# Kernel optimization log

Hardware: AMD Instinct MI355X
Metric: run time of the kernel (lower is better)

## Reference

```python
import jax, jax.numpy as jnp
import numpy as np

B, T, I, H, C = 128, 1024, 256, 512, 10


def setup_inputs() -> dict:
    key = jax.random.key(0)
    ks = jax.random.split(key, 11)
    s1 = 1.0 / np.sqrt(H)
    u = lambda k, shp, s: jax.random.uniform(k, shp, jnp.float32, -s, s)
    return {
        "x": jax.random.normal(ks[0], (B, T, I), jnp.float32),
        "w_ih1": u(ks[1], (H, I), s1),
        "w_hh1": u(ks[2], (H, H), s1),
        "b_ih1": u(ks[3], (H,), s1),
        "b_hh1": u(ks[4], (H,), s1),
        "w_ih2": u(ks[5], (H, H), s1),
        "w_hh2": u(ks[6], (H, H), s1),
        "b_ih2": u(ks[7], (H,), s1),
        "b_hh2": u(ks[8], (H,), s1),
        "w_out": u(ks[9], (C, H), s1),
        "b_out": u(ks[10], (C,), s1),
    }


def reference(x, w_ih1, w_hh1, b_ih1, b_hh1, w_ih2, w_hh2, b_ih2, b_hh2, w_out, b_out):
    batch = x.shape[0]
    h0 = jnp.zeros((batch, H), x.dtype)

    def step(carry, x_t):
        h1, h2 = carry
        # cell 1: tanh(x_t @ w_ih1^T + b_ih1 + h1 @ w_hh1^T + b_hh1)
        h1 = jnp.tanh(x_t @ w_ih1.T + b_ih1 + h1 @ w_hh1.T + b_hh1)
        # cell 2 takes h1 as input
        h2 = jnp.tanh(h1 @ w_ih2.T + b_ih2 + h2 @ w_hh2.T + b_hh2)
        return (h1, h2), None

    # scan over time: x transposed to [T, B, I]
    (h1_T, h2_T), _ = jax.lax.scan(step, (h0, h0), jnp.swapaxes(x, 0, 1))
    return h2_T @ w_out.T + b_out
```

## Files before the change

kernel.cpp:

```cpp
#include <hip/hip_runtime.h>
#include <hip/hip_fp16.h>

#define Tt 1024
#define Ii 256
#define Hh 512
#define Cc 10
#define SPINMAX (1 << 27)

typedef _Float16 f16;
typedef _Float16 f16x8 __attribute__((ext_vector_type(8)));
typedef _Float16 f16x4 __attribute__((ext_vector_type(4)));
typedef _Float16 f16x2 __attribute__((ext_vector_type(2)));
typedef float    f32x4 __attribute__((ext_vector_type(4)));

#define OFF_FLAGS 0u
#define OFF_WH1   4096u
#define OFF_WH2   528384u
#define OFF_XWR   1052672u
#define OFF_H1R   3149824u
#define OFF_PAR   4198400u

static __device__ __forceinline__ f32x4 mfma16(f16x8 a, f16x8 b, f32x4 c) {
  return __builtin_amdgcn_mfma_f32_16x16x32_f16(a, b, c, 0, 0, 0);
}
static __device__ __forceinline__ float fast_tanh(float v) {
  float e = __expf(2.0f * v);
  return 1.0f - 2.0f / (e + 1.0f);
}
static __device__ __forceinline__ int ldflag(const int* p) {
  return __hip_atomic_load(p, __ATOMIC_RELAXED, __HIP_MEMORY_SCOPE_AGENT);
}
static __device__ __forceinline__ void stflag(int* p, int v) {
  __hip_atomic_store(p, v, __ATOMIC_RELAXED, __HIP_MEMORY_SCOPE_AGENT);
}
static __device__ __forceinline__ f16x4 ld64cc(const f16* p) {
  union { unsigned long long u; f16x4 v; } U;
  U.u = __hip_atomic_load((const unsigned long long*)p, __ATOMIC_RELAXED, __HIP_MEMORY_SCOPE_AGENT);
  return U.v;
}
static __device__ __forceinline__ void st64cc(f16* p, f16x4 v) {
  union { unsigned long long u; f16x4 v; } U; U.v = v;
  __hip_atomic_store((unsigned long long*)p, U.u, __ATOMIC_RELAXED, __HIP_MEMORY_SCOPE_AGENT);
}
static __device__ __forceinline__ f16x8 ld128cc(const f16* p) {
  union { unsigned long long u[2]; f16x8 v; } U;
  U.u[0] = __hip_atomic_load((const unsigned long long*)p,     __ATOMIC_RELAXED, __HIP_MEMORY_SCOPE_AGENT);
  U.u[1] = __hip_atomic_load((const unsigned long long*)p + 1, __ATOMIC_RELAXED, __HIP_MEMORY_SCOPE_AGENT);
  return U.v;
}
static __device__ __forceinline__ void stu32cc(unsigned* p, unsigned v) {
  __hip_atomic_store(p, v, __ATOMIC_RELAXED, __HIP_MEMORY_SCOPE_AGENT);
}
static __device__ __forceinline__ int imin(int a, int b) { return a < b ? a : b; }

#define CFENCE() asm volatile("" ::: "memory")
#define VMFENCE() asm volatile("s_waitcnt vmcnt(0)" ::: "memory")
#define LBAR() do { asm volatile("s_waitcnt lgkmcnt(0)" ::: "memory"); \
                    __builtin_amdgcn_s_barrier(); \
                    __builtin_amdgcn_sched_barrier(0); } while (0)

__global__ void prep_weights(const float* __restrict__ w_hh1,
                             const float* __restrict__ w_hh2,
                             char* __restrict__ ws) {
  f16* wh1 = (f16*)(ws + OFF_WH1);
  f16* wh2 = (f16*)(ws + OFF_WH2);
  int i = blockIdx.x * 512 + threadIdx.x;
  if (i < 512 * 512) { wh1[i] = (f16)w_hh1[i]; wh2[i] = (f16)w_hh2[i]; }
}

__global__ __launch_bounds__(512, 1) void rnn_main(
    const float* __restrict__ x,
    const float* __restrict__ w_ih1, const float* __restrict__ w_ih2,
    const float* __restrict__ b_ih1, const float* __restrict__ b_hh1,
    const float* __restrict__ b_ih2, const float* __restrict__ b_hh2,
    const float* __restrict__ w_out, const float* __restrict__ b_out,
    float* __restrict__ out, char* __restrict__ ws)
{
  __shared__ __align__(16) char LS[147712];

  int* FL = (int*)(ws + OFF_FLAGS);
  const f16* wh1f = (const f16*)(ws + OFF_WH1);
  const f16* wh2f = (const f16*)(ws + OFF_WH2);
  f16* xwr = (f16*)(ws + OFF_XWR);
  f16* h1r = (f16*)(ws + OFF_H1R);
  f16* parr = (f16*)(ws + OFF_PAR);

  const int bid  = blockIdx.x;
  const int tid  = threadIdx.x;
  const int wid  = tid >> 6;
  const int lane = tid & 63;
  const int lm   = lane & 15;
  const int lgrp = lane >> 4;
  const int lk8  = lgrp * 8;
  const int rlo  = (lane & 1) * 2;

  if (bid < 16) {
    const bool isH1 = (bid < 8);
    const int bg = bid & 7;
    f16* sB = (f16*)LS;
    f16* sH = (f16*)(LS + 131072);
    unsigned* sH32 = (unsigned*)sH;
    const f16* whh = isH1 ? wh1f : wh2f;
    const int wcol0 = wid * 64;

    for (int i = tid; i < 8192; i += 512) {
      const int kc = i >> 11, grp = (i >> 9) & 3, col = i & 511;
      f16x8 v = *(const f16x8*)&whh[col * 512 + kc * 32 + grp * 8];
      *(f16x8*)&sB[(size_t)i * 8] = v;
    }
    for (int i = tid; i < 16 * 260; i += 512) sH32[i] = 0u;
    f16x8 wb[12][4];
    #pragma unroll
    for (int kr = 0; kr < 12; ++kr)
      #pragma unroll
      for (int nt = 0; nt < 4; ++nt)
        wb[kr][nt] = *(const f16x8*)&whh[(size_t)(wcol0 + nt * 16 + lm) * 512 + (kr + 4) * 32 + lk8];
    __syncthreads();

    int fA_cur = -1;
    int fG_cur = -1;
    const int T = Tt;

    for (int p = 0; p < T; ++p) {
      if (isH1) {
        if (fA_cur < p + 1) {
          const int* pa = FL + 32 + (bg * 2 + (p & 1)) * 2;
          int s = 0, a, b;
          do { a = ldflag(pa); b = ldflag(pa + 1); if (++s > SPINMAX) break; }
          while (imin(a, b) < p + 1);
        }
        if (p >= 8 && fG_cur < p - 7) {
          const int sg = (p - 8) % 3;
          const int* qa = FL + 96 + (bg * 3 + sg) * 4;
          int s = 0, m;
          do { m = imin(imin(ldflag(qa), ldflag(qa + 1)), imin(ldflag(qa + 2), ldflag(qa + 3)));
               if (++s > SPINMAX) break; } while (m < p - 7);
        }
      } else {
        if (fA_cur < p + 1) {
          const int sg = p % 3;
          const int* qa = FL + 96 + (bg * 3 + sg) * 4;
          int s = 0, m;
          do { m = imin(imin(ldflag(qa), ldflag(qa + 1)), imin(ldflag(qa + 2), ldflag(qa + 3)));
               if (++s > SPINMAX) break; } while (m < p + 1);
        }
      }
      CFENCE();

      const f16* fin = isH1 ? (xwr + ((size_t)(p & 15) * 8 + bg) * 8192)
                            : (parr + ((size_t)(p & 7) * 8 + bg) * 8192);
      f16x4 xv[4];
      #pragma unroll
      for (int nt = 0; nt < 4; ++nt)
        xv[nt] = ld64cc(fin + (wid * 4 + nt) * 256 + lm * 16 + lgrp * 4);

      f32x4 acc[4];
      #pragma unroll
      for (int nt = 0; nt < 4; ++nt) acc[nt] = f32x4{0.f, 0.f, 0.f, 0.f};
      if (p > 0) {
        #pragma unroll
        for (int kc = 0; kc < 16; ++kc) {
          f16x8 A = *(const f16x8*)&sH[lm * 520 + kc * 32 + lk8];
          if (kc < 4) {
            #pragma unroll
            for (int nt = 0; nt < 4; ++nt)
              acc[nt] = mfma16(A, *(const f16x8*)&sB[((size_t)(kc * 4 + lgrp) * 512 + wcol0 + nt * 16 + lm) * 8], acc[nt]);
          } else {
            #pragma unroll
            for (int nt = 0; nt < 4; ++nt)
              acc[nt] = mfma16(A, wb[kc - 4][nt], acc[nt]);
          }
        }
      }
      LBAR();

      #pragma unroll
      for (int nt = 0; nt < 4; ++nt) {
        #pragma unroll
        for (int r = 0; r < 4; ++r) acc[nt][r] += (float)xv[nt][r];
      }

      if ((p & 3) == 0 && p > 0) {
        VMFENCE();
        if (tid == 0) stflag(FL + (isH1 ? 0 : 16) + bg, p);
      }

      unsigned* ring32 = (unsigned*)(h1r + ((size_t)(p & 7) * 8 + bg) * 8192);
      #pragma unroll
      for (int nt = 0; nt < 4; ++nt) {
        const int cp = (wcol0 + nt * 16 + lm) >> 1;
        float v0 = fast_tanh(acc[nt][0]), v1 = fast_tanh(acc[nt][1]);
        float v2 = fast_tanh(acc[nt][2]), v3 = fast_tanh(acc[nt][3]);
        float o0 = __shfl_xor(v0, 1, 64), o1 = __shfl_xor(v1, 1, 64);
        float o2 = __shfl_xor(v2, 1, 64), o3 = __shfl_xor(v3, 1, 64);
        float m[4] = {v0, v1, v2, v3}, q[4] = {o0, o1, o2, o3};
        #pragma unroll
        for (int r2 = 0; r2 < 2; ++r2) {
          const int rr = rlo + r2, row = lgrp * 4 + rr;
          float ve = (lane & 1) ? q[rr] : m[rr];
          float vo = (lane & 1) ? m[rr] : q[rr];
          union { f16x2 h; unsigned u; } P; P.h = f16x2{(f16)ve, (f16)vo};
          sH32[row * 260 + cp] = P.u;
          if (isH1) stu32cc(ring32 + row * 256 + cp, P.u);
        }
      }

      if (isH1) {
        const int* pa = FL + 32 + (bg * 2 + ((p + 1) & 1)) * 2;
        fA_cur = imin(ldflag(pa), ldflag(pa + 1));
        const int sg2 = (p + 1 >= 8) ? ((p - 7) % 3) : 0;
        const int* qa = FL + 96 + (bg * 3 + sg2) * 4;
        fG_cur = imin(imin(ldflag(qa), ldflag(qa + 1)), imin(ldflag(qa + 2), ldflag(qa + 3)));
      } else {
        const int sg2 = (p + 1) % 3;
        const int* qa = FL + 96 + (bg * 3 + sg2) * 4;
        fA_cur = imin(imin(ldflag(qa), ldflag(qa + 1)), imin(ldflag(qa + 2), ldflag(qa + 3)));
      }

      LBAR();
    }

    VMFENCE();
    if (tid == 0) stflag(FL + (isH1 ? 0 : 16) + bg, Tt);
    if (tid == 0 && isH1) stflag(FL + bg, Tt + 1);
    if (tid == 0 && !isH1) stflag(FL + 16 + bg, Tt + 1);

    if (!isH1) {
      const int rl = wid * 2 + (lane >> 5);
      const int l32 = lane & 31;
      const f16* hr = &sH[rl * 520 + l32 * 16];
      f16x8 h0 = *(const f16x8*)hr;
      f16x8 h1v = *(const f16x8*)(hr + 8);
      float hf[16];
      #pragma unroll
      for (int j = 0; j < 8; ++j) { hf[j] = (float)h0[j]; hf[8 + j] = (float)h1v[j]; }
      #pragma unroll
      for (int c = 0; c < Cc; ++c) {
        const float* wr_ = w_out + (size_t)c * Hh + l32 * 16;
        float s = 0.f;
        #pragma unroll
        for (int j4 = 0; j4 < 4; ++j4) {
          float4 w4 = *(const float4*)(wr_ + j4 * 4);
          s += hf[j4*4]*w4.x + hf[j4*4+1]*w4.y + hf[j4*4+2]*w4.z + hf[j4*4+3]*w4.w;
        }
        #pragma unroll
        for (int off = 16; off >= 1; off >>= 1) s += __shfl_xor(s, off, 64);
        if (l32 == 0) out[(bg * 16 + rl) * Cc + c] = s + b_out[c];
      }
    }
  } else if (bid < 112) {
    const int idx = bid - 16;
    const int bg = idx / 12, r = idx % 12;
    const int set = r >> 2, cb = r & 3;
    f16* sW = (f16*)LS;
    f16* sA = (f16*)(LS + 131072);

    for (int i = tid; i < 8192; i += 512) {
      const int kc = i >> 9, grp = (i >> 7) & 3, cl = i & 127;
      const float* sp = w_ih2 + (size_t)(cb * 128 + cl) * 512 + kc * 32 + grp * 8;
      float4 a = *(const float4*)sp, b = *(const float4*)(sp + 4);
      f16x8 v{(f16)a.x,(f16)a.y,(f16)a.z,(f16)a.w,(f16)b.x,(f16)b.y,(f16)b.z,(f16)b.w};
      *(f16x8*)&sW[(size_t)i * 8] = v;
    }
    const int gcol = cb * 128 + wid * 16 + lm;
    const float bias2v = b_ih2[gcol] + b_hh2[gcol];
    __syncthreads();

    for (int q = set; q < Tt; q += 3) {
      if (q >= 8) {
        int s = 0;
        while (ldflag(FL + 16 + bg) < q - 7) { if (++s > SPINMAX) break; __builtin_amdgcn_s_sleep(1); }
      }
      { int s = 0;
        while (ldflag(FL + bg) < q + 1) { if (++s > SPINMAX) break; __builtin_amdgcn_s_sleep(1); } }
      CFENCE();
      const f16* hsrc = h1r + ((size_t)(q & 7) * 8 + bg) * 8192;
      #pragma unroll
      for (int c = 0; c < 2; ++c) {
        const int ch = tid * 2 + c;
        const int row = ch >> 6, c16 = ch & 63;
        f16x8 v = ld128cc(hsrc + ch * 8);
        *(f16x8*)&sA[row * 520 + c16 * 8] = v;
      }
      __syncthreads();
      f32x4 acc = {bias2v, bias2v, bias2v, bias2v};
      #pragma unroll
      for (int kc = 0; kc < 16; ++kc) {
        f16x8 A = *(const f16x8*)&sA[lm * 520 + kc * 32 + lk8];
        f16x8 B = *(const f16x8*)&sW[((size_t)(kc * 4 + lgrp) * 128 + wid * 16 + lm) * 8];
        acc = mfma16(A, B, acc);
      }
      f16x4 pv{(f16)acc[0], (f16)acc[1], (f16)acc[2], (f16)acc[3]};
      st64cc(parr + ((size_t)(q & 7) * 8 + bg) * 8192 + (cb * 8 + wid) * 256 + lm * 16 + lgrp * 4, pv);
      VMFENCE();
      if (tid == 0) stflag(FL + 96 + (bg * 3 + set) * 4 + cb, q + 1);
      __syncthreads();
    }
  } else {
    const int idx = bid - 112;
    const int bg = idx >> 2, r = idx & 3;
    const int set = r >> 1, half = r & 1;
    f16* sW = (f16*)LS;

    for (int i = tid; i < 8192; i += 512) {
      const int kc = i >> 10, grp = (i >> 8) & 3, cl = i & 255;
      const float* sp = w_ih1 + (size_t)(half * 256 + cl) * 256 + kc * 32 + grp * 8;
      float4 a = *(const float4*)sp, b = *(const float4*)(sp + 4);
      f16x8 v{(f16)a.x,(f16)a.y,(f16)a.z,(f16)a.w,(f16)b.x,(f16)b.y,(f16)b.z,(f16)b.w};
      *(f16x8*)&sW[(size_t)i * 8] = v;
    }
    const int gc0 = half * 256 + wid * 32 + lm;
    const float b1v0 = b_ih1[gc0] + b_hh1[gc0];
    const float b1v1 = b_ih1[gc0 + 16] + b_hh1[gc0 + 16];
    __syncthreads();

    for (int t = set; t < Tt; t += 2) {
      if (t >= 16) {
        int s = 0;
        while (ldflag(FL + bg) < t - 15) { if (++s > SPINMAX) break; __builtin_amdgcn_s_sleep(1); }
      }
      CFENCE();
      f32x4 acc0 = {b1v0, b1v0, b1v0, b1v0};
      f32x4 acc1 = {b1v1, b1v1, b1v1, b1v1};
      const float* xr = x + ((size_t)(bg * 16 + lm) * Tt + t) * Ii + lk8;
      #pragma unroll
      for (int kc = 0; kc < 8; ++kc) {
        float4 a = *(const float4*)(xr + kc * 32);
        float4 b = *(const float4*)(xr + kc * 32 + 4);
        f16x8 A{(f16)a.x,(f16)a.y,(f16)a.z,(f16)a.w,(f16)b.x,(f16)b.y,(f16)b.z,(f16)b.w};
        acc0 = mfma16(A, *(const f16x8*)&sW[((size_t)(kc * 4 + lgrp) * 256 + wid * 32 + lm) * 8], acc0);
        acc1 = mfma16(A, *(const f16x8*)&sW[((size_t)(kc * 4 + lgrp) * 256 + wid * 32 + 16 + lm) * 8], acc1);
      }
      f16* dst = xwr + ((size_t)(t & 15) * 8 + bg) * 8192;
      f16x4 p0{(f16)acc0[0], (f16)acc0[1], (f16)acc0[2], (f16)acc0[3]};
      f16x4 p1{(f16)acc1[0], (f16)acc1[1], (f16)acc1[2], (f16)acc1[3]};
      st64cc(dst + (half * 16 + wid * 2 + 0) * 256 + lm * 16 + lgrp * 4, p0);
      st64cc(dst + (half * 16 + wid * 2 + 1) * 256 + lm * 16 + lgrp * 4, p1);
      VMFENCE();
      if (tid == 0) stflag(FL + 32 + (bg * 2 + set) * 2 + half, t + 1);
    }
  }
}

extern "C" void kernel_launch(void* const* d_in, const int* in_sizes, int n_in,
                              void* d_out, int out_size, void* d_ws, size_t ws_size,
                              hipStream_t stream) {
  (void)in_sizes; (void)n_in; (void)out_size; (void)ws_size;
  const float* x     = (const float*)d_in[0];
  const float* w_ih1 = (const float*)d_in[1];
  const float* w_hh1 = (const float*)d_in[2];
  const float* b_ih1 = (const float*)d_in[3];
  const float* b_hh1 = (const float*)d_in[4];
  const float* w_ih2 = (const float*)d_in[5];
  const float* w_hh2 = (const float*)d_in[6];
  const float* b_ih2 = (const float*)d_in[7];
  const float* b_hh2 = (const float*)d_in[8];
  const float* w_out = (const float*)d_in[9];
  const float* b_out = (const float*)d_in[10];
  float* out = (float*)d_out;
  char* ws = (char*)d_ws;

  hipMemsetAsync(ws, 0, 4096, stream);
  hipLaunchKernelGGL(prep_weights, dim3(512), dim3(512), 0, stream, w_hh1, w_hh2, ws);
  hipLaunchKernelGGL(rnn_main, dim3(144), dim3(512), 0, stream,
                     x, w_ih1, w_ih2, b_ih1, b_hh1, b_ih2, b_hh2,
                     w_out, b_out, out, ws);
}
```

Baseline: 7.353 ms.

## Restructure RNN producer-consumer pipeline with deeper rings and prefetched feeds

Reworks the cross-block dataflow schedule. The x-projection gets three producer sets per batch group and the grid grows to 160 blocks. Ring buffers deepen from 8 to 16 slots, the recurrent blocks prefetch the next step's input feed before the tanh phase, and the layer-2 input-projection blocks prefetch their next h1 tile into registers. The register-cached w_hh slice is dropped in favour of direct global (cache) loads inside the MFMA loop, which frees registers but adds memory latency on the critical recurrence path. Flag layout and handshake semantics are redesigned, and spin loops now bail out with a dead flag.

```diff
diff --git a/kernel.cpp b/kernel.cpp
--- a/kernel.cpp
+++ b/kernel.cpp
@@ -5,7 +5,7 @@
 #define Ii 256
 #define Hh 512
 #define Cc 10
-#define SPINMAX (1 << 27)
+#define SPINMAX (1 << 24)
 
 typedef _Float16 f16;
 typedef _Float16 f16x8 __attribute__((ext_vector_type(8)));
@@ -13,12 +13,16 @@
 typedef _Float16 f16x2 __attribute__((ext_vector_type(2)));
 typedef float    f32x4 __attribute__((ext_vector_type(4)));
 
-#define OFF_FLAGS 0u
 #define OFF_WH1   4096u
 #define OFF_WH2   528384u
 #define OFF_XWR   1052672u
 #define OFF_H1R   3149824u
-#define OFF_PAR   4198400u
+#define OFF_PAR   5246976u
+
+#define FI_H1 0
+#define FI_H2 16
+#define FI_XW 128
+#define FI_2A 256
 
 static __device__ __forceinline__ f32x4 mfma16(f16x8 a, f16x8 b, f32x4 c) {
   return __builtin_amdgcn_mfma_f32_16x16x32_f16(a, b, c, 0, 0, 0);
@@ -53,7 +57,6 @@
 }
 static __device__ __forceinline__ int imin(int a, int b) { return a < b ? a : b; }
 
-#define CFENCE() asm volatile("" ::: "memory")
 #define VMFENCE() asm volatile("s_waitcnt vmcnt(0)" ::: "memory")
 #define LBAR() do { asm volatile("s_waitcnt lgkmcnt(0)" ::: "memory"); \
                     __builtin_amdgcn_s_barrier(); \
@@ -78,11 +81,11 @@
 {
   __shared__ __align__(16) char LS[147712];
 
-  int* FL = (int*)(ws + OFF_FLAGS);
+  int* FL = (int*)ws;
   const f16* wh1f = (const f16*)(ws + OFF_WH1);
   const f16* wh2f = (const f16*)(ws + OFF_WH2);
-  f16* xwr = (f16*)(ws + OFF_XWR);
-  f16* h1r = (f16*)(ws + OFF_H1R);
+  f16* xwr  = (f16*)(ws + OFF_XWR);
+  f16* h1r  = (f16*)(ws + OFF_H1R);
   f16* parr = (f16*)(ws + OFF_PAR);
 
   const int bid  = blockIdx.x;
@@ -105,54 +108,68 @@
 
     for (int i = tid; i < 8192; i += 512) {
       const int kc = i >> 11, grp = (i >> 9) & 3, col = i & 511;
-      f16x8 v = *(const f16x8*)&whh[col * 512 + kc * 32 + grp * 8];
-      *(f16x8*)&sB[(size_t)i * 8] = v;
+      *(f16x8*)&sB[(size_t)i * 8] =
+        *(const f16x8*)&whh[(size_t)col * 512 + kc * 32 + grp * 8];
     }
     for (int i = tid; i < 16 * 260; i += 512) sH32[i] = 0u;
-    f16x8 wb[12][4];
-    #pragma unroll
-    for (int kr = 0; kr < 12; ++kr)
+    __syncthreads();
+
+    const int* pfxw = FL + FI_XW + bg * 6;
+    const int* pf2a = FL + FI_2A + bg * 12;
+    int dead = 0;
+    bool have = true;
+    f16x4 fvc[4], fvn[4];
+    int cfeed, cg = 0;
+
+    if (isH1) {
+      int v, sp = 0;
+      do { v = imin(ldflag(pfxw + 0), ldflag(pfxw + 1));
+           if (++sp > SPINMAX) { dead = 1; break; } } while (v < 1);
+      const f16* fs = xwr + (size_t)bg * 8192;
       #pragma unroll
       for (int nt = 0; nt < 4; ++nt)
-        wb[kr][nt] = *(const f16x8*)&whh[(size_t)(wcol0 + nt * 16 + lm) * 512 + (kr + 4) * 32 + lk8];
-    __syncthreads();
-
-    int fA_cur = -1;
-    int fG_cur = -1;
-    const int T = Tt;
-
-    for (int p = 0; p < T; ++p) {
-      if (isH1) {
-        if (fA_cur < p + 1) {
-          const int* pa = FL + 32 + (bg * 2 + (p & 1)) * 2;
-          int s = 0, a, b;
-          do { a = ldflag(pa); b = ldflag(pa + 1); if (++s > SPINMAX) break; }
-          while (imin(a, b) < p + 1);
-        }
-        if (p >= 8 && fG_cur < p - 7) {
-          const int sg = (p - 8) % 3;
-          const int* qa = FL + 96 + (bg * 3 + sg) * 4;
-          int s = 0, m;
-          do { m = imin(imin(ldflag(qa), ldflag(qa + 1)), imin(ldflag(qa + 2), ldflag(qa + 3)));
-               if (++s > SPINMAX) break; } while (m < p - 7);
-        }
-      } else {
-        if (fA_cur < p + 1) {
-          const int sg = p % 3;
-          const int* qa = FL + 96 + (bg * 3 + sg) * 4;
-          int s = 0, m;
-          do { m = imin(imin(ldflag(qa), ldflag(qa + 1)), imin(ldflag(qa + 2), ldflag(qa + 3)));
-               if (++s > SPINMAX) break; } while (m < p + 1);
-        }
-      }
-      CFENCE();
-
-      const f16* fin = isH1 ? (xwr + ((size_t)(p & 15) * 8 + bg) * 8192)
-                            : (parr + ((size_t)(p & 7) * 8 + bg) * 8192);
-      f16x4 xv[4];
+        fvc[nt] = ld64cc(fs + (wid * 4 + nt) * 256 + lm * 16 + lgrp * 4);
+      cfeed = imin(ldflag(pfxw + 1 * 2), ldflag(pfxw + 1 * 2 + 1));
+    } else {
+      int v, sp = 0;
+      do { v = imin(imin(ldflag(pf2a + 0), ldflag(pf2a + 1)),
+                    imin(ldflag(pf2a + 2), ldflag(pf2a + 3)));
+           if (++sp > SPINMAX) { dead = 1; break; } } while (v < 1);
+      const f16* fs = parr + (size_t)bg * 8192;
       #pragma unroll
       for (int nt = 0; nt < 4; ++nt)
-        xv[nt] = ld64cc(fin + (wid * 4 + nt) * 256 + lm * 16 + lgrp * 4);
+        fvc[nt] = ld64cc(fs + (wid * 4 + nt) * 256 + lm * 16 + lgrp * 4);
+      cfeed = imin(imin(ldflag(pf2a + 4), ldflag(pf2a + 5)),
+                   imin(ldflag(pf2a + 6), ldflag(pf2a + 7)));
+    }
+
+    for (int p = 0; p < Tt && !dead; ++p) {
+      if (!have) {
+        if (isH1) {
+          const int s = p % 3; int v, sp = 0;
+          do { v = imin(ldflag(pfxw + s * 2), ldflag(pfxw + s * 2 + 1));
+               if (++sp > SPINMAX) { dead = 1; break; } } while (v < p + 1);
+          const f16* fs = xwr + ((size_t)(p & 15) * 8 + bg) * 8192;
+          #pragma unroll
+          for (int nt = 0; nt < 4; ++nt)
+            fvc[nt] = ld64cc(fs + (wid * 4 + nt) * 256 + lm * 16 + lgrp * 4);
+        } else {
+          const int sg = p % 3; int v, sp = 0;
+          do { v = imin(imin(ldflag(pf2a + sg*4), ldflag(pf2a + sg*4+1)),
+                        imin(ldflag(pf2a + sg*4+2), ldflag(pf2a + sg*4+3)));
+               if (++sp > SPINMAX) { dead = 1; break; } } while (v < p + 1);
+          const f16* fs = parr + ((size_t)(p & 15) * 8 + bg) * 8192;
+          #pragma unroll
+          for (int nt = 0; nt < 4; ++nt)
+            fvc[nt] = ld64cc(fs + (wid * 4 + nt) * 256 + lm * 16 + lgrp * 4);
+        }
+      }
+      if (isH1 && p >= 16 && cg < p - 15) {
+        const int sg = (p - 16) % 3; int v, sp = 0;
+        do { v = imin(imin(ldflag(pf2a + sg*4), ldflag(pf2a + sg*4+1)),
+                      imin(ldflag(pf2a + sg*4+2), ldflag(pf2a + sg*4+3)));
+             if (++sp > SPINMAX) { dead = 1; break; } } while (v < p - 15);
+      }
 
       f32x4 acc[4];
       #pragma unroll
@@ -164,41 +181,51 @@
           if (kc < 4) {
             #pragma unroll
             for (int nt = 0; nt < 4; ++nt)
-              acc[nt] = mfma16(A, *(const f16x8*)&sB[((size_t)(kc * 4 + lgrp) * 512 + wcol0 + nt * 16 + lm) * 8], acc[nt]);
+              acc[nt] = mfma16(A, *(const f16x8*)&sB[((size_t)(kc*4+lgrp)*512 + wcol0 + nt*16 + lm)*8], acc[nt]);
           } else {
             #pragma unroll
             for (int nt = 0; nt < 4; ++nt)
-              acc[nt] = mfma16(A, wb[kc - 4][nt], acc[nt]);
+              acc[nt] = mfma16(A, *(const f16x8*)&whh[(size_t)(wcol0+nt*16+lm)*512 + kc*32 + lk8], acc[nt]);
           }
         }
       }
       LBAR();
 
       #pragma unroll
-      for (int nt = 0; nt < 4; ++nt) {
-        #pragma unroll
-        for (int r = 0; r < 4; ++r) acc[nt][r] += (float)xv[nt][r];
-      }
-
-      if ((p & 3) == 0 && p > 0) {
+      for (int nt = 0; nt < 4; ++nt)
+        #pragma unroll
+        for (int r = 0; r < 4; ++r) acc[nt][r] += (float)fvc[nt][r];
+
+      if (isH1) {
         VMFENCE();
-        if (tid == 0) stflag(FL + (isH1 ? 0 : 16) + bg, p);
-      }
-
-      unsigned* ring32 = (unsigned*)(h1r + ((size_t)(p & 7) * 8 + bg) * 8192);
+        if (tid == 0) stflag(FL + FI_H1 + bg, p);
+      } else {
+        if (tid == 0) stflag(FL + FI_H2 + bg, p + 1);
+      }
+
+      have = false;
+      if (p + 1 < Tt && cfeed >= p + 2) {
+        const f16* fs = (isH1 ? xwr : parr) + ((size_t)((p + 1) & 15) * 8 + bg) * 8192;
+        #pragma unroll
+        for (int nt = 0; nt < 4; ++nt)
+          fvn[nt] = ld64cc(fs + (wid * 4 + nt) * 256 + lm * 16 + lgrp * 4);
+        have = true;
+      }
+
+      unsigned* ring32 = (unsigned*)(h1r + ((size_t)(p & 15) * 8 + bg) * 8192);
       #pragma unroll
       for (int nt = 0; nt < 4; ++nt) {
         const int cp = (wcol0 + nt * 16 + lm) >> 1;
         float v0 = fast_tanh(acc[nt][0]), v1 = fast_tanh(acc[nt][1]);
         float v2 = fast_tanh(acc[nt][2]), v3 = fast_tanh(acc[nt][3]);
-        float o0 = __shfl_xor(v0, 1, 64), o1 = __shfl_xor(v1, 1, 64);
-        float o2 = __shfl_xor(v2, 1, 64), o3 = __shfl_xor(v3, 1, 64);
-        float m[4] = {v0, v1, v2, v3}, q[4] = {o0, o1, o2, o3};
+        float o0 = __shfl_xor(v0,1,64), o1 = __shfl_xor(v1,1,64);
+        float o2 = __shfl_xor(v2,1,64), o3 = __shfl_xor(v3,1,64);
+        float m[4] = {v0,v1,v2,v3}, qd[4] = {o0,o1,o2,o3};
         #pragma unroll
         for (int r2 = 0; r2 < 2; ++r2) {
           const int rr = rlo + r2, row = lgrp * 4 + rr;
-          float ve = (lane & 1) ? q[rr] : m[rr];
-          float vo = (lane & 1) ? m[rr] : q[rr];
+          float ve = (lane & 1) ? qd[rr] : m[rr];
+          float vo = (lane & 1) ? m[rr] : qd[rr];
           union { f16x2 h; unsigned u; } P; P.h = f16x2{(f16)ve, (f16)vo};
           sH32[row * 260 + cp] = P.u;
           if (isH1) stu32cc(ring32 + row * 256 + cp, P.u);
@@ -206,24 +233,27 @@
       }
 
       if (isH1) {
-        const int* pa = FL + 32 + (bg * 2 + ((p + 1) & 1)) * 2;
-        fA_cur = imin(ldflag(pa), ldflag(pa + 1));
-        const int sg2 = (p + 1 >= 8) ? ((p - 7) % 3) : 0;
-        const int* qa = FL + 96 + (bg * 3 + sg2) * 4;
-        fG_cur = imin(imin(ldflag(qa), ldflag(qa + 1)), imin(ldflag(qa + 2), ldflag(qa + 3)));
+        const int s2 = (p + 2) % 3;
+        cfeed = imin(ldflag(pfxw + s2*2), ldflag(pfxw + s2*2 + 1));
+        if (p + 1 >= 16) {
+          const int sg = (p + 1 - 16) % 3;
+          cg = imin(imin(ldflag(pf2a + sg*4), ldflag(pf2a + sg*4+1)),
+                    imin(ldflag(pf2a + sg*4+2), ldflag(pf2a + sg*4+3)));
+        }
       } else {
-        const int sg2 = (p + 1) % 3;
-        const int* qa = FL + 96 + (bg * 3 + sg2) * 4;
-        fA_cur = imin(imin(ldflag(qa), ldflag(qa + 1)), imin(ldflag(qa + 2), ldflag(qa + 3)));
-      }
-
+        const int sg2 = (p + 2) % 3;
+        cfeed = imin(imin(ldflag(pf2a + sg2*4), ldflag(pf2a + sg2*4+1)),
+                     imin(ldflag(pf2a + sg2*4+2), ldflag(pf2a + sg2*4+3)));
+      }
       LBAR();
+      if (have) {
+        #pragma unroll
+        for (int nt = 0; nt < 4; ++nt) fvc[nt] = fvn[nt];
+      }
     }
 
     VMFENCE();
-    if (tid == 0) stflag(FL + (isH1 ? 0 : 16) + bg, Tt);
-    if (tid == 0 && isH1) stflag(FL + bg, Tt + 1);
-    if (tid == 0 && !isH1) stflag(FL + 16 + bg, Tt + 1);
+    if (tid == 0) stflag(FL + (isH1 ? FI_H1 : FI_H2) + bg, Tt + 2);
 
     if (!isH1) {
       const int rl = wid * 2 + (lane >> 5);
@@ -250,8 +280,8 @@
     }
   } else if (bid < 112) {
     const int idx = bid - 16;
-    const int bg = idx / 12, r = idx % 12;
-    const int set = r >> 2, cb = r & 3;
+    const int bg = idx / 12, r12 = idx % 12;
+    const int set = r12 >> 2, cb = r12 & 3;
     f16* sW = (f16*)LS;
     f16* sA = (f16*)(LS + 131072);
 
@@ -259,30 +289,34 @@
       const int kc = i >> 9, grp = (i >> 7) & 3, cl = i & 127;
       const float* sp = w_ih2 + (size_t)(cb * 128 + cl) * 512 + kc * 32 + grp * 8;
       float4 a = *(const float4*)sp, b = *(const float4*)(sp + 4);
-      f16x8 v{(f16)a.x,(f16)a.y,(f16)a.z,(f16)a.w,(f16)b.x,(f16)b.y,(f16)b.z,(f16)b.w};
-      *(f16x8*)&sW[(size_t)i * 8] = v;
+      *(f16x8*)&sW[(size_t)i * 8] =
+        f16x8{(f16)a.x,(f16)a.y,(f16)a.z,(f16)a.w,(f16)b.x,(f16)b.y,(f16)b.z,(f16)b.w};
     }
     const int gcol = cb * 128 + wid * 16 + lm;
     const float bias2v = b_ih2[gcol] + b_hh2[gcol];
     __syncthreads();
 
-    for (int q = set; q < Tt; q += 3) {
-      if (q >= 8) {
-        int s = 0;
-        while (ldflag(FL + 16 + bg) < q - 7) { if (++s > SPINMAX) break; __builtin_amdgcn_s_sleep(1); }
-      }
-      { int s = 0;
-        while (ldflag(FL + bg) < q + 1) { if (++s > SPINMAX) break; __builtin_amdgcn_s_sleep(1); } }
-      CFENCE();
-      const f16* hsrc = h1r + ((size_t)(q & 7) * 8 + bg) * 8192;
-      #pragma unroll
-      for (int c = 0; c < 2; ++c) {
-        const int ch = tid * 2 + c;
-        const int row = ch >> 6, c16 = ch & 63;
-        f16x8 v = ld128cc(hsrc + ch * 8);
-        *(f16x8*)&sA[row * 520 + c16 * 8] = v;
-      }
-      __syncthreads();
+    int* myf = FL + FI_2A + (bg * 3 + set) * 4 + cb;
+    const int row_ = tid >> 5, c32 = tid & 31;
+    int dead = 0;
+    f16x8 R0, R1;
+    {
+      int v, sp = 0;
+      do { v = ldflag(FL + FI_H1 + bg); if (++sp > SPINMAX) { dead = 1; break; } }
+      while (v < set + 1);
+      const f16* hs = h1r + ((size_t)(set & 15) * 8 + bg) * 8192;
+      R0 = ld128cc(hs + (size_t)tid * 16);
+      R1 = ld128cc(hs + (size_t)tid * 16 + 8);
+    }
+    int cfh1 = ldflag(FL + FI_H1 + bg);
+    int cfh2 = ldflag(FL + FI_H2 + bg);
+
+    for (int q = set; q < Tt && !dead; q += 3) {
+      VMFENCE();
+      if (q >= 3 && tid == 0) stflag(myf, q - 2);
+      *(f16x8*)&sA[row_ * 520 + c32 * 16]     = R0;
+      *(f16x8*)&sA[row_ * 520 + c32 * 16 + 8] = R1;
+      LBAR();
       f32x4 acc = {bias2v, bias2v, bias2v, bias2v};
       #pragma unroll
       for (int kc = 0; kc < 16; ++kc) {
@@ -290,36 +324,55 @@
         f16x8 B = *(const f16x8*)&sW[((size_t)(kc * 4 + lgrp) * 128 + wid * 16 + lm) * 8];
         acc = mfma16(A, B, acc);
       }
-      f16x4 pv{(f16)acc[0], (f16)acc[1], (f16)acc[2], (f16)acc[3]};
-      st64cc(parr + ((size_t)(q & 7) * 8 + bg) * 8192 + (cb * 8 + wid) * 256 + lm * 16 + lgrp * 4, pv);
-      VMFENCE();
-      if (tid == 0) stflag(FL + 96 + (bg * 3 + set) * 4 + cb, q + 1);
+      st64cc(parr + ((size_t)(q & 15) * 8 + bg) * 8192 + (cb * 8 + wid) * 256 + lm * 16 + lgrp * 4,
+             f16x4{(f16)acc[0], (f16)acc[1], (f16)acc[2], (f16)acc[3]});
+      if (q + 3 < Tt) {
+        if (cfh1 < q + 4) {
+          int v, sp = 0;
+          do { v = ldflag(FL + FI_H1 + bg); if (++sp > SPINMAX) { dead = 1; break; } }
+          while (v < q + 4);
+        }
+        if (q + 3 >= 16 && cfh2 < q - 12) {
+          int v, sp = 0;
+          do { v = ldflag(FL + FI_H2 + bg); if (++sp > SPINMAX) { dead = 1; break; } }
+          while (v < q - 12);
+        }
+        const f16* hs = h1r + ((size_t)((q + 3) & 15) * 8 + bg) * 8192;
+        R0 = ld128cc(hs + (size_t)tid * 16);
+        R1 = ld128cc(hs + (size_t)tid * 16 + 8);
+      }
+      cfh1 = ldflag(FL + FI_H1 + bg);
+      cfh2 = ldflag(FL + FI_H2 + bg);
       __syncthreads();
     }
+    VMFENCE();
+    if (tid == 0) stflag(myf, Tt + 2);
   } else {
     const int idx = bid - 112;
-    const int bg = idx >> 2, r = idx & 3;
-    const int set = r >> 1, half = r & 1;
+    const int bg = idx / 6, r6 = idx % 6;
+    const int set = r6 >> 1, half = r6 & 1;
     f16* sW = (f16*)LS;
 
     for (int i = tid; i < 8192; i += 512) {
       const int kc = i >> 10, grp = (i >> 8) & 3, cl = i & 255;
       const float* sp = w_ih1 + (size_t)(half * 256 + cl) * 256 + kc * 32 + grp * 8;
       float4 a = *(const float4*)sp, b = *(const float4*)(sp + 4);
-      f16x8 v{(f16)a.x,(f16)a.y,(f16)a.z,(f16)a.w,(f16)b.x,(f16)b.y,(f16)b.z,(f16)b.w};
-      *(f16x8*)&sW[(size_t)i * 8] = v;
+      *(f16x8*)&sW[(size_t)i * 8] =
+        f16x8{(f16)a.x,(f16)a.y,(f16)a.z,(f16)a.w,(f16)b.x,(f16)b.y,(f16)b.z,(f16)b.w};
     }
     const int gc0 = half * 256 + wid * 32 + lm;
     const float b1v0 = b_ih1[gc0] + b_hh1[gc0];
     const float b1v1 = b_ih1[gc0 + 16] + b_hh1[gc0 + 16];
     __syncthreads();
 
-    for (int t = set; t < Tt; t += 2) {
-      if (t >= 16) {
-        int s = 0;
-        while (ldflag(FL + bg) < t - 15) { if (++s > SPINMAX) break; __builtin_amdgcn_s_sleep(1); }
-      }
-      CFENCE();
+    int* myf = FL + FI_XW + (bg * 3 + set) * 2 + half;
+    int cfh1 = 0, dead = 0;
+    for (int t = set; t < Tt && !dead; t += 3) {
+      if (t >= 16 && cfh1 < t - 15) {
+        int v, sp = 0;
+        do { v = ldflag(FL + FI_H1 + bg); if (++sp > SPINMAX) { dead = 1; break; } }
+        while (v < t - 15);
+      }
       f32x4 acc0 = {b1v0, b1v0, b1v0, b1v0};
       f32x4 acc1 = {b1v1, b1v1, b1v1, b1v1};
       const float* xr = x + ((size_t)(bg * 16 + lm) * Tt + t) * Ii + lk8;
@@ -328,17 +381,19 @@
         float4 a = *(const float4*)(xr + kc * 32);
         float4 b = *(const float4*)(xr + kc * 32 + 4);
         f16x8 A{(f16)a.x,(f16)a.y,(f16)a.z,(f16)a.w,(f16)b.x,(f16)b.y,(f16)b.z,(f16)b.w};
-        acc0 = mfma16(A, *(const f16x8*)&sW[((size_t)(kc * 4 + lgrp) * 256 + wid * 32 + lm) * 8], acc0);
-        acc1 = mfma16(A, *(const f16x8*)&sW[((size_t)(kc * 4 + lgrp) * 256 + wid * 32 + 16 + lm) * 8], acc1);
+        acc0 = mfma16(A, *(const f16x8*)&sW[((size_t)(kc*4+lgrp)*256 + wid*32 + lm)*8], acc0);
+        acc1 = mfma16(A, *(const f16x8*)&sW[((size_t)(kc*4+lgrp)*256 + wid*32 + 16 + lm)*8], acc1);
       }
       f16* dst = xwr + ((size_t)(t & 15) * 8 + bg) * 8192;
-      f16x4 p0{(f16)acc0[0], (f16)acc0[1], (f16)acc0[2], (f16)acc0[3]};
-      f16x4 p1{(f16)acc1[0], (f16)acc1[1], (f16)acc1[2], (f16)acc1[3]};
-      st64cc(dst + (half * 16 + wid * 2 + 0) * 256 + lm * 16 + lgrp * 4, p0);
-      st64cc(dst + (half * 16 + wid * 2 + 1) * 256 + lm * 16 + lgrp * 4, p1);
+      st64cc(dst + (half*16 + wid*2 + 0)*256 + lm*16 + lgrp*4,
+             f16x4{(f16)acc0[0],(f16)acc0[1],(f16)acc0[2],(f16)acc0[3]});
+      st64cc(dst + (half*16 + wid*2 + 1)*256 + lm*16 + lgrp*4,
+             f16x4{(f16)acc1[0],(f16)acc1[1],(f16)acc1[2],(f16)acc1[3]});
       VMFENCE();
-      if (tid == 0) stflag(FL + 32 + (bg * 2 + set) * 2 + half, t + 1);
-    }
+      if (tid == 0) stflag(myf, t + 1);
+      cfh1 = ldflag(FL + FI_H1 + bg);
+    }
+    if (tid == 0) stflag(myf, Tt + 2);
   }
 }
 
@@ -362,7 +417,7 @@
 
   hipMemsetAsync(ws, 0, 4096, stream);
   hipLaunchKernelGGL(prep_weights, dim3(512), dim3(512), 0, stream, w_hh1, w_hh2, ws);
-  hipLaunchKernelGGL(rnn_main, dim3(144), dim3(512), 0, stream,
+  hipLaunchKernelGGL(rnn_main, dim3(160), dim3(512), 0, stream,
                      x, w_ih1, w_ih2, b_ih1, b_hh1, b_ih2, b_hh2,
                      w_out, b_out, out, ws);
 }
```

Measured after the change: 16.47 ms. +124.0%, slower.

## Pin recurrent weights in AGPRs and stream last K-chunks from global memory

Applied to the files above, without the earlier changes.

The recurrent weight slice kept in registers shrinks from 12 to 8 K-chunks, and an empty inline asm constraint pins those 8 chunks to accumulator registers (AGPRs). The last 4 K-chunks are now reloaded from global memory (L2-cached) on every timestep, issued in two batches so the loads overlap with the MFMAs. This is meant to relieve VGPR pressure or spilling in the persistent recurrence kernel. The cost is extra global loads on the latency-critical serial path of each step.

```diff
diff --git a/kernel.cpp b/kernel.cpp
--- a/kernel.cpp
+++ b/kernel.cpp
@@ -109,12 +109,15 @@
       *(f16x8*)&sB[(size_t)i * 8] = v;
     }
     for (int i = tid; i < 16 * 260; i += 512) sH32[i] = 0u;
-    f16x8 wb[12][4];
+    f16x8 wbA[8][4];
     #pragma unroll
-    for (int kr = 0; kr < 12; ++kr)
-      #pragma unroll
-      for (int nt = 0; nt < 4; ++nt)
-        wb[kr][nt] = *(const f16x8*)&whh[(size_t)(wcol0 + nt * 16 + lm) * 512 + (kr + 4) * 32 + lk8];
+    for (int kr = 0; kr < 8; ++kr) {
+      #pragma unroll
+      for (int nt = 0; nt < 4; ++nt) {
+        wbA[kr][nt] = *(const f16x8*)&whh[(size_t)(wcol0 + nt * 16 + lm) * 512 + (kr + 4) * 32 + lk8];
+        asm volatile("" : "+a"(wbA[kr][nt]));
+      }
+    }
     __syncthreads();
 
     int fA_cur = -1;
@@ -158,17 +161,29 @@
       #pragma unroll
       for (int nt = 0; nt < 4; ++nt) acc[nt] = f32x4{0.f, 0.f, 0.f, 0.f};
       if (p > 0) {
+        f16x8 ws[4][4];
+        #pragma unroll
+        for (int g = 0; g < 2; ++g)
+          #pragma unroll
+          for (int nt = 0; nt < 4; ++nt)
+            ws[g][nt] = *(const f16x8*)&whh[(size_t)(wcol0 + nt * 16 + lm) * 512 + (12 + g) * 32 + lk8];
         #pragma unroll
         for (int kc = 0; kc < 16; ++kc) {
+          if (kc == 8) {
+            #pragma unroll
+            for (int g = 2; g < 4; ++g)
+              #pragma unroll
+              for (int nt = 0; nt < 4; ++nt)
+                ws[g][nt] = *(const f16x8*)&whh[(size_t)(wcol0 + nt * 16 + lm) * 512 + (12 + g) * 32 + lk8];
+          }
           f16x8 A = *(const f16x8*)&sH[lm * 520 + kc * 32 + lk8];
-          if (kc < 4) {
-            #pragma unroll
-            for (int nt = 0; nt < 4; ++nt)
-              acc[nt] = mfma16(A, *(const f16x8*)&sB[((size_t)(kc * 4 + lgrp) * 512 + wcol0 + nt * 16 + lm) * 8], acc[nt]);
-          } else {
-            #pragma unroll
-            for (int nt = 0; nt < 4; ++nt)
-              acc[nt] = mfma16(A, wb[kc - 4][nt], acc[nt]);
+          #pragma unroll
+          for (int nt = 0; nt < 4; ++nt) {
+            f16x8 B;
+            if (kc < 4)       B = *(const f16x8*)&sB[((size_t)(kc * 4 + lgrp) * 512 + wcol0 + nt * 16 + lm) * 8];
+            else if (kc < 12) B = wbA[kc - 4][nt];
+            else              B = ws[kc - 12][nt];
+            acc[nt] = mfma16(A, B, acc[nt]);
           }
         }
       }
```

Measured after the change: 9.624 ms. 30.9% more time.

## Deepen inter-block rings to 16 slots and prefetch h1 in projection blocks

Applied to the files above, without the earlier changes.

Grows the h1 and projection ring buffers from 8 to 16 slots, which loosens the producer/consumer back-pressure between the recurrent blocks and the layer-2 input-projection blocks. The projection blocks now load the next h1 tile into registers before waiting, and they publish progress flags earlier. The recurrent blocks read the next step's readiness flags earlier in the step, overlapping those reads with the MFMA work, and they publish progress every 2 steps instead of every 4. The cost is a larger workspace and more flag traffic, with some added risk of protocol errors in the reworked flag semantics.

```diff
diff --git a/kernel.cpp b/kernel.cpp
--- a/kernel.cpp
+++ b/kernel.cpp
@@ -18,7 +18,7 @@
 #define OFF_WH2   528384u
 #define OFF_XWR   1052672u
 #define OFF_H1R   3149824u
-#define OFF_PAR   4198400u
+#define OFF_PAR   5246976u
 
 static __device__ __forceinline__ f32x4 mfma16(f16x8 a, f16x8 b, f32x4 c) {
   return __builtin_amdgcn_mfma_f32_16x16x32_f16(a, b, c, 0, 0, 0);
@@ -117,27 +117,26 @@
         wb[kr][nt] = *(const f16x8*)&whh[(size_t)(wcol0 + nt * 16 + lm) * 512 + (kr + 4) * 32 + lk8];
     __syncthreads();
 
-    int fA_cur = -1;
-    int fG_cur = -1;
-    const int T = Tt;
-
-    for (int p = 0; p < T; ++p) {
+    int rF0 = -1, rF1 = -1, rF2 = -1, rF3 = -1;
+    int rG0 = -1, rG1 = -1, rG2 = -1, rG3 = -1;
+
+    for (int p = 0; p < Tt; ++p) {
       if (isH1) {
-        if (fA_cur < p + 1) {
+        if (imin(rF0, rF1) < p + 1) {
           const int* pa = FL + 32 + (bg * 2 + (p & 1)) * 2;
           int s = 0, a, b;
           do { a = ldflag(pa); b = ldflag(pa + 1); if (++s > SPINMAX) break; }
           while (imin(a, b) < p + 1);
         }
-        if (p >= 8 && fG_cur < p - 7) {
-          const int sg = (p - 8) % 3;
+        if (p >= 16 && imin(imin(rG0, rG1), imin(rG2, rG3)) < p - 15) {
+          const int sg = (p - 16) % 3;
           const int* qa = FL + 96 + (bg * 3 + sg) * 4;
           int s = 0, m;
           do { m = imin(imin(ldflag(qa), ldflag(qa + 1)), imin(ldflag(qa + 2), ldflag(qa + 3)));
-               if (++s > SPINMAX) break; } while (m < p - 7);
+               if (++s > SPINMAX) break; } while (m < p - 15);
         }
       } else {
-        if (fA_cur < p + 1) {
+        if (imin(imin(rF0, rF1), imin(rF2, rF3)) < p + 1) {
           const int sg = p % 3;
           const int* qa = FL + 96 + (bg * 3 + sg) * 4;
           int s = 0, m;
@@ -148,11 +147,25 @@
       CFENCE();
 
       const f16* fin = isH1 ? (xwr + ((size_t)(p & 15) * 8 + bg) * 8192)
-                            : (parr + ((size_t)(p & 7) * 8 + bg) * 8192);
+                            : (parr + ((size_t)(p & 15) * 8 + bg) * 8192);
       f16x4 xv[4];
       #pragma unroll
       for (int nt = 0; nt < 4; ++nt)
         xv[nt] = ld64cc(fin + (wid * 4 + nt) * 256 + lm * 16 + lgrp * 4);
+
+      if (isH1) {
+        const int* pa = FL + 32 + (bg * 2 + ((p + 1) & 1)) * 2;
+        rF0 = ldflag(pa); rF1 = ldflag(pa + 1);
+        if (p + 1 >= 16) {
+          const int* qa = FL + 96 + (bg * 3 + ((p - 15) % 3)) * 4;
+          rG0 = ldflag(qa); rG1 = ldflag(qa + 1);
+          rG2 = ldflag(qa + 2); rG3 = ldflag(qa + 3);
+        }
+      } else {
+        const int* qa = FL + 96 + (bg * 3 + ((p + 1) % 3)) * 4;
+        rF0 = ldflag(qa); rF1 = ldflag(qa + 1);
+        rF2 = ldflag(qa + 2); rF3 = ldflag(qa + 3);
+      }
 
       f32x4 acc[4];
       #pragma unroll
@@ -180,12 +193,12 @@
         for (int r = 0; r < 4; ++r) acc[nt][r] += (float)xv[nt][r];
       }
 
-      if ((p & 3) == 0 && p > 0) {
+      if ((p & 1) == 0 && p > 0) {
         VMFENCE();
         if (tid == 0) stflag(FL + (isH1 ? 0 : 16) + bg, p);
       }
 
-      unsigned* ring32 = (unsigned*)(h1r + ((size_t)(p & 7) * 8 + bg) * 8192);
+      unsigned* ring32 = (unsigned*)(h1r + ((size_t)(p & 15) * 8 + bg) * 8192);
       #pragma unroll
       for (int nt = 0; nt < 4; ++nt) {
         const int cp = (wcol0 + nt * 16 + lm) >> 1;
@@ -205,25 +218,11 @@
         }
       }
 
-      if (isH1) {
-        const int* pa = FL + 32 + (bg * 2 + ((p + 1) & 1)) * 2;
-        fA_cur = imin(ldflag(pa), ldflag(pa + 1));
-        const int sg2 = (p + 1 >= 8) ? ((p - 7) % 3) : 0;
-        const int* qa = FL + 96 + (bg * 3 + sg2) * 4;
-        fG_cur = imin(imin(ldflag(qa), ldflag(qa + 1)), imin(ldflag(qa + 2), ldflag(qa + 3)));
-      } else {
-        const int sg2 = (p + 1) % 3;
-        const int* qa = FL + 96 + (bg * 3 + sg2) * 4;
-        fA_cur = imin(imin(ldflag(qa), ldflag(qa + 1)), imin(ldflag(qa + 2), ldflag(qa + 3)));
-      }
-
       LBAR();
     }
 
     VMFENCE();
-    if (tid == 0) stflag(FL + (isH1 ? 0 : 16) + bg, Tt);
-    if (tid == 0 && isH1) stflag(FL + bg, Tt + 1);
-    if (tid == 0 && !isH1) stflag(FL + 16 + bg, Tt + 1);
+    if (tid == 0) stflag(FL + (isH1 ? 0 : 16) + bg, Tt + 2);
 
     if (!isH1) {
       const int rl = wid * 2 + (lane >> 5);
@@ -266,22 +265,25 @@
     const float bias2v = b_ih2[gcol] + b_hh2[gcol];
     __syncthreads();
 
-    for (int q = set; q < Tt; q += 3) {
-      if (q >= 8) {
-        int s = 0;
-        while (ldflag(FL + 16 + bg) < q - 7) { if (++s > SPINMAX) break; __builtin_amdgcn_s_sleep(1); }
-      }
-      { int s = 0;
-        while (ldflag(FL + bg) < q + 1) { if (++s > SPINMAX) break; __builtin_amdgcn_s_sleep(1); } }
-      CFENCE();
-      const f16* hsrc = h1r + ((size_t)(q & 7) * 8 + bg) * 8192;
-      #pragma unroll
-      for (int c = 0; c < 2; ++c) {
-        const int ch = tid * 2 + c;
-        const int row = ch >> 6, c16 = ch & 63;
-        f16x8 v = ld128cc(hsrc + ch * 8);
-        *(f16x8*)&sA[row * 520 + c16 * 8] = v;
-      }
+    int* myf = FL + 96 + (bg * 3 + set) * 4 + cb;
+    const int* fH1 = FL + bg;
+    const int* fH2 = FL + 16 + bg;
+    int dead = 0;
+    f16x8 R0, R1;
+    {
+      int s = 0;
+      while (ldflag(fH1) < set + 1) { if (++s > SPINMAX) { dead = 1; break; } __builtin_amdgcn_s_sleep(1); }
+      const f16* hs = h1r + ((size_t)(set & 15) * 8 + bg) * 8192;
+      R0 = ld128cc(hs + (size_t)tid * 16);
+      R1 = ld128cc(hs + (size_t)tid * 16 + 8);
+    }
+    int rH1 = ldflag(fH1), rH2 = ldflag(fH2);
+
+    for (int q = set; q < Tt && !dead; q += 3) {
+      VMFENCE();
+      if (q >= 3 && tid == 0) stflag(myf, q - 2);
+      *(f16x8*)&sA[(tid >> 5) * 520 + (tid & 31) * 16]     = R0;
+      *(f16x8*)&sA[(tid >> 5) * 520 + (tid & 31) * 16 + 8] = R1;
       __syncthreads();
       f32x4 acc = {bias2v, bias2v, bias2v, bias2v};
       #pragma unroll
@@ -290,12 +292,30 @@
         f16x8 B = *(const f16x8*)&sW[((size_t)(kc * 4 + lgrp) * 128 + wid * 16 + lm) * 8];
         acc = mfma16(A, B, acc);
       }
-      f16x4 pv{(f16)acc[0], (f16)acc[1], (f16)acc[2], (f16)acc[3]};
-      st64cc(parr + ((size_t)(q & 7) * 8 + bg) * 8192 + (cb * 8 + wid) * 256 + lm * 16 + lgrp * 4, pv);
-      VMFENCE();
-      if (tid == 0) stflag(FL + 96 + (bg * 3 + set) * 4 + cb, q + 1);
+      if (q >= 16 && rH2 < q - 15) {
+        int s = 0, v;
+        do { v = ldflag(fH2); if (v >= q - 15) break;
+             __builtin_amdgcn_s_sleep(1); } while (++s < SPINMAX);
+        if (v < q - 15) dead = 1;
+      }
+      st64cc(parr + ((size_t)(q & 15) * 8 + bg) * 8192 + (cb * 8 + wid) * 256 + lm * 16 + lgrp * 4,
+             f16x4{(f16)acc[0], (f16)acc[1], (f16)acc[2], (f16)acc[3]});
+      if (q + 3 < Tt) {
+        if (rH1 < q + 4) {
+          int s = 0, v;
+          do { v = ldflag(fH1); if (v >= q + 4) break;
+               __builtin_amdgcn_s_sleep(1); } while (++s < SPINMAX);
+          if (v < q + 4) dead = 1;
+        }
+        const f16* hs = h1r + ((size_t)((q + 3) & 15) * 8 + bg) * 8192;
+        R0 = ld128cc(hs + (size_t)tid * 16);
+        R1 = ld128cc(hs + (size_t)tid * 16 + 8);
+      }
+      rH1 = ldflag(fH1); rH2 = ldflag(fH2);
       __syncthreads();
     }
+    VMFENCE();
+    if (tid == 0) stflag(myf, Tt + 2);
   } else {
     const int idx = bid - 112;
     const int bg = idx >> 2, r = idx & 3;
@@ -339,6 +359,7 @@
       VMFENCE();
       if (tid == 0) stflag(FL + 32 + (bg * 2 + set) * 2 + half, t + 1);
     }
+    if (tid == 0) stflag(FL + 32 + (bg * 2 + set) * 2 + half, Tt + 2);
   }
 }
 
```

Result: slower. 8.115 ms (+10.4%).
